# Kernel optimization log

Hardware: AMD Instinct MI355X
Metric: run time of the kernel (lower is better)

The kernel has to match this reference:

```python
import jax, jax.numpy as jnp
import numpy as np

SHIFT = 1e-09  # input_shift


def _patches(v, kh, kw):
    # v: (B, C, H, W) -> (B, C, kh*kw, Ho, Wo), VALID padding, stride 1
    B, C, H, W = v.shape
    Ho, Wo = H - kh + 1, W - kw + 1
    cols = [v[:, :, i:i + Ho, j:j + Wo] for i in range(kh) for j in range(kw)]
    return jnp.stack(cols, axis=2)


def setup_inputs() -> dict:
    key = jax.random.key(0)
    kx, k1k, k2k, kb = jax.random.split(key, 4)
    B, C, H, W = 32, 64, 64, 64
    kh, kw, F = 3, 3, 128
    x = jax.random.normal(kx, (B, C, H, W), dtype=jnp.float32)
    # log-domain kernels (learned params of the two Add modules)
    k1 = jax.random.normal(k1k, (kh, kw, C, F), dtype=jnp.float32) * 0.1
    k2 = jax.random.normal(k2k, (kh, kw, C, F), dtype=jnp.float32) * 0.1
    bias = jnp.zeros((F,), dtype=jnp.float32)
    return {"x": x, "k1": k1, "k2": k2, "bias": bias}


def reference(x, k1, k2, bias):
    kh, kw, C, F = k1.shape
    # Ln: log of ReLU'd patches (positive and negative parts of x)
    ep_pos = jnp.exp(jnp.log(jax.nn.relu(_patches(x, kh, kw)) + SHIFT))   # (B,C,kh*kw,Ho,Wo)
    ep_neg = jnp.exp(jnp.log(jax.nn.relu(_patches(-x, kh, kw)) + SHIFT))
    # Add + Exp + patch reduction: sum_p exp(ln_patch + k) == einsum(exp(ln_patch), exp(k))
    ek1 = jnp.exp(k1).reshape(kh * kw, C, F)
    ek2 = jnp.exp(k2).reshape(kh * kw, C, F)
    y11 = jnp.einsum('bckhw,kcf->bfhw', ep_pos, ek1)
    y12 = jnp.einsum('bckhw,kcf->bfhw', ep_pos, ek2)
    y21 = jnp.einsum('bckhw,kcf->bfhw', ep_neg, ek1)
    y22 = jnp.einsum('bckhw,kcf->bfhw', ep_neg, ek2)
    return y11 - y12 - y21 + y22 + bias[None, :, None, None]
```

## Files before the change

kernel.cpp:

```cpp
#include <hip/hip_runtime.h>
#include <hip/hip_bf16.h>

typedef __attribute__((ext_vector_type(4))) float f32x4;
typedef __attribute__((ext_vector_type(8))) short bf16x8;

static __device__ __forceinline__ unsigned short f2bf(float f) {
    unsigned int u = __float_as_uint(f);
    unsigned int r = (u + 0x7FFFu + ((u >> 16) & 1u)) >> 16;
    return (unsigned short)r;
}

__global__ __launch_bounds__(256) void wprep_kernel(const float* __restrict__ k1,
                                                    const float* __restrict__ k2,
                                                    unsigned short* __restrict__ wp) {
    int idx = blockIdx.x * 256 + threadIdx.x;
    if (idx >= 9 * 128 * 64) return;
    int c = idx & 63;
    int f = (idx >> 6) & 127;
    int p = idx >> 13;
    int src = (p * 64 + c) * 128 + f;
    float v = expf(k1[src]) - expf(k2[src]);
    wp[idx] = f2bf(v);
}

__global__ __launch_bounds__(256, 3) void conv_kernel(const float* __restrict__ x,
                                                      const unsigned short* __restrict__ wp,
                                                      const float* __restrict__ bias,
                                                      float* __restrict__ out) {
    __shared__ unsigned short xs[4 * 64 * 64];
    __shared__ unsigned short bs[128 * 64];

    int bid0 = blockIdx.x;
    int bid  = (bid0 & 7) * 124 + (bid0 >> 3);
    int b    = bid / 31;
    int tile = bid - b * 31;
    int oh0  = tile * 2;

    int tid  = threadIdx.x;
    int lane = tid & 63;
    const float* xb = x + b * (64 * 4096);
    const uint4* wp16 = (const uint4*)wp;

    uint4 wreg[4];
#pragma unroll
    for (int i2 = 0; i2 < 4; ++i2) wreg[i2] = wp16[i2 * 256 + tid];

    {
        int col = tid & 63;
        int u0  = tid >> 6;
#pragma unroll
        for (int j = 0; j < 8; ++j) {
            int u   = u0 + j * 4;
            int row = u >> 3;
            int cg  = u & 7;
            float v[8];
#pragma unroll
            for (int e = 0; e < 8; ++e)
                v[e] = xb[(cg * 8 + e) * 4096 + (oh0 + row) * 64 + col];
            uint4 pk;
            pk.x = (unsigned int)f2bf(v[0]) | ((unsigned int)f2bf(v[1]) << 16);
            pk.y = (unsigned int)f2bf(v[2]) | ((unsigned int)f2bf(v[3]) << 16);
            pk.z = (unsigned int)f2bf(v[4]) | ((unsigned int)f2bf(v[5]) << 16);
            pk.w = (unsigned int)f2bf(v[6]) | ((unsigned int)f2bf(v[7]) << 16);
            *(uint4*)(&xs[((row * 64 + col) << 6) + ((cg * 8) ^ ((col & 7) << 3))]) = pk;
        }
    }

    int wid = tid >> 6;
    int wr  = wid >> 1;
    int wc  = wid & 1;
    int lr  = lane & 15;
    int lk8 = (lane >> 4) << 3;

    f32x4 acc[4][4];
#pragma unroll
    for (int ni = 0; ni < 4; ++ni)
#pragma unroll
        for (int mi = 0; mi < 4; ++mi) acc[ni][mi] = (f32x4){0.f, 0.f, 0.f, 0.f};

#pragma unroll
    for (int p = 0; p < 9; ++p) {
        __syncthreads();
#pragma unroll
        for (int i2 = 0; i2 < 4; ++i2) {
            int q = i2 * 256 + tid;
            int f = q >> 3, cc = q & 7;
            *(uint4*)(&bs[f * 64 + ((cc * 8) ^ ((f & 7) << 3))]) = wreg[i2];
        }
        if (p < 8) {
#pragma unroll
            for (int i2 = 0; i2 < 4; ++i2) wreg[i2] = wp16[(p + 1) * 1024 + i2 * 256 + tid];
        }
        __syncthreads();
        const int ki = p / 3, kj = p % 3;
#pragma unroll
        for (int kb = 0; kb < 64; kb += 32) {
            int c0 = kb + lk8;
            bf16x8 af[4], bfr[4];
#pragma unroll
            for (int mi = 0; mi < 4; ++mi) {
                int col  = mi * 16 + lr + kj;
                int colc = col > 63 ? 63 : col;
                af[mi] = *(const bf16x8*)(&xs[(((wr + ki) * 64 + colc) << 6) + (c0 ^ ((colc & 7) << 3))]);
            }
#pragma unroll
            for (int ni = 0; ni < 4; ++ni) {
                int f = wc * 64 + ni * 16 + lr;
                bfr[ni] = *(const bf16x8*)(&bs[f * 64 + (c0 ^ ((f & 7) << 3))]);
            }
#pragma unroll
            for (int ni = 0; ni < 4; ++ni)
#pragma unroll
                for (int mi = 0; mi < 4; ++mi)
                    acc[ni][mi] = __builtin_amdgcn_mfma_f32_16x16x32_bf16(bfr[ni], af[mi], acc[ni][mi], 0, 0, 0);
        }
    }

    int oh = oh0 + wr;
    float* ob = out + b * (128 * 62 * 62);
#pragma unroll
    for (int ni = 0; ni < 4; ++ni) {
        int fb = wc * 64 + ni * 16 + ((lane >> 4) << 2);
        f32x4 bv4 = *(const f32x4*)(bias + fb);
#pragma unroll
        for (int t = 0; t < 4; ++t) {
            int f = fb + t;
            float* orow = ob + (f * 62 + oh) * 62;
#pragma unroll
            for (int mi = 0; mi < 4; ++mi) {
                int ow = mi * 16 + lr;
                if (ow < 62) orow[ow] = acc[ni][mi][t] + bv4[t];
            }
        }
    }
}

extern "C" void kernel_launch(void* const* d_in, const int* in_sizes, int n_in,
                              void* d_out, int out_size, void* d_ws, size_t ws_size,
                              hipStream_t stream) {
    const float* x    = (const float*)d_in[0];
    const float* k1   = (const float*)d_in[1];
    const float* k2   = (const float*)d_in[2];
    const float* bias = (const float*)d_in[3];
    float* out = (float*)d_out;

    unsigned short* wp = (unsigned short*)d_ws;

    hipLaunchKernelGGL(wprep_kernel, dim3(288), dim3(256), 0, stream, k1, k2, wp);
    hipLaunchKernelGGL(conv_kernel, dim3(992), dim3(256), 0, stream, x, wp, bias, out);
}
```

Measured before the change: 138.2 us.

## Load weight MFMA fragments directly from global into registers, drop LDS staging

The weight prep kernel now writes weights in a fragment-friendly layout (per tap, per half of the channel range, filter-major with 32 channels contiguous). Each lane of the conv kernel can then load its MFMA B operands straight from global or L2 into registers, double-buffered across the 9 taps. This removes the shared weight buffer and the two block barriers per tap. In exchange, each wave issues redundant global loads of the same weights and uses more registers, which may hurt occupancy.

```diff
diff --git a/kernel.cpp b/kernel.cpp
--- a/kernel.cpp
+++ b/kernel.cpp
@@ -4,31 +4,30 @@
 typedef __attribute__((ext_vector_type(4))) float f32x4;
 typedef __attribute__((ext_vector_type(8))) short bf16x8;
 
-static __device__ __forceinline__ unsigned short f2bf(float f) {
+static __device__ __forceinline__ unsigned int f2bf(float f) {
     unsigned int u = __float_as_uint(f);
-    unsigned int r = (u + 0x7FFFu + ((u >> 16) & 1u)) >> 16;
-    return (unsigned short)r;
+    return (u + 0x7FFFu + ((u >> 16) & 1u)) >> 16;
 }
 
 __global__ __launch_bounds__(256) void wprep_kernel(const float* __restrict__ k1,
                                                     const float* __restrict__ k2,
-                                                    unsigned short* __restrict__ wp) {
+                                                    unsigned short* __restrict__ wq) {
     int idx = blockIdx.x * 256 + threadIdx.x;
-    if (idx >= 9 * 128 * 64) return;
-    int c = idx & 63;
-    int f = (idx >> 6) & 127;
-    int p = idx >> 13;
-    int src = (p * 64 + c) * 128 + f;
+    if (idx >= 73728) return;
+    int f  = idx & 127;
+    int ch = (idx >> 7) & 31;
+    int kh = (idx >> 12) & 1;
+    int p  = idx >> 13;
+    int src = (p * 64 + kh * 32 + ch) * 128 + f;
     float v = expf(k1[src]) - expf(k2[src]);
-    wp[idx] = f2bf(v);
+    wq[((p * 2 + kh) * 128 + f) * 32 + ch] = (unsigned short)f2bf(v);
 }
 
 __global__ __launch_bounds__(256, 3) void conv_kernel(const float* __restrict__ x,
-                                                      const unsigned short* __restrict__ wp,
+                                                      const unsigned short* __restrict__ wq,
                                                       const float* __restrict__ bias,
                                                       float* __restrict__ out) {
     __shared__ unsigned short xs[4 * 64 * 64];
-    __shared__ unsigned short bs[128 * 64];
 
     int bid0 = blockIdx.x;
     int bid  = (bid0 & 7) * 124 + (bid0 >> 3);
@@ -38,19 +37,19 @@
 
     int tid  = threadIdx.x;
     int lane = tid & 63;
+    int wid  = tid >> 6;
+    int wr   = wid >> 1;
+    int wc   = wid & 1;
+    int lr   = lane & 15;
+    int hi   = lane >> 4;
+
     const float* xb = x + b * (64 * 4096);
-    const uint4* wp16 = (const uint4*)wp;
-
-    uint4 wreg[4];
-#pragma unroll
-    for (int i2 = 0; i2 < 4; ++i2) wreg[i2] = wp16[i2 * 256 + tid];
 
     {
         int col = tid & 63;
-        int u0  = tid >> 6;
 #pragma unroll
         for (int j = 0; j < 8; ++j) {
-            int u   = u0 + j * 4;
+            int u   = wid + j * 4;
             int row = u >> 3;
             int cg  = u & 7;
             float v[8];
@@ -58,19 +57,22 @@
             for (int e = 0; e < 8; ++e)
                 v[e] = xb[(cg * 8 + e) * 4096 + (oh0 + row) * 64 + col];
             uint4 pk;
-            pk.x = (unsigned int)f2bf(v[0]) | ((unsigned int)f2bf(v[1]) << 16);
-            pk.y = (unsigned int)f2bf(v[2]) | ((unsigned int)f2bf(v[3]) << 16);
-            pk.z = (unsigned int)f2bf(v[4]) | ((unsigned int)f2bf(v[5]) << 16);
-            pk.w = (unsigned int)f2bf(v[6]) | ((unsigned int)f2bf(v[7]) << 16);
+            pk.x = f2bf(v[0]) | (f2bf(v[1]) << 16);
+            pk.y = f2bf(v[2]) | (f2bf(v[3]) << 16);
+            pk.z = f2bf(v[4]) | (f2bf(v[5]) << 16);
+            pk.w = f2bf(v[6]) | (f2bf(v[7]) << 16);
             *(uint4*)(&xs[((row * 64 + col) << 6) + ((cg * 8) ^ ((col & 7) << 3))]) = pk;
         }
     }
 
-    int wid = tid >> 6;
-    int wr  = wid >> 1;
-    int wc  = wid & 1;
-    int lr  = lane & 15;
-    int lk8 = (lane >> 4) << 3;
+    const bf16x8* wg = (const bf16x8*)wq;
+    int fb0 = wc * 64 + lr;
+    bf16x8 wfrag[2][8];
+#pragma unroll
+    for (int kh = 0; kh < 2; ++kh)
+#pragma unroll
+        for (int ni = 0; ni < 4; ++ni)
+            wfrag[0][kh * 4 + ni] = wg[((kh) * 128 + fb0 + ni * 16) * 4 + hi];
 
     f32x4 acc[4][4];
 #pragma unroll
@@ -78,25 +80,23 @@
 #pragma unroll
         for (int mi = 0; mi < 4; ++mi) acc[ni][mi] = (f32x4){0.f, 0.f, 0.f, 0.f};
 
+    __syncthreads();
+
 #pragma unroll
     for (int p = 0; p < 9; ++p) {
-        __syncthreads();
-#pragma unroll
-        for (int i2 = 0; i2 < 4; ++i2) {
-            int q = i2 * 256 + tid;
-            int f = q >> 3, cc = q & 7;
-            *(uint4*)(&bs[f * 64 + ((cc * 8) ^ ((f & 7) << 3))]) = wreg[i2];
-        }
+        const int cur = p & 1, nxt = cur ^ 1;
         if (p < 8) {
 #pragma unroll
-            for (int i2 = 0; i2 < 4; ++i2) wreg[i2] = wp16[(p + 1) * 1024 + i2 * 256 + tid];
+            for (int kh = 0; kh < 2; ++kh)
+#pragma unroll
+                for (int ni = 0; ni < 4; ++ni)
+                    wfrag[nxt][kh * 4 + ni] = wg[(((p + 1) * 2 + kh) * 128 + fb0 + ni * 16) * 4 + hi];
         }
-        __syncthreads();
         const int ki = p / 3, kj = p % 3;
 #pragma unroll
-        for (int kb = 0; kb < 64; kb += 32) {
-            int c0 = kb + lk8;
-            bf16x8 af[4], bfr[4];
+        for (int kb = 0; kb < 2; ++kb) {
+            int c0 = kb * 32 + hi * 8;
+            bf16x8 af[4];
 #pragma unroll
             for (int mi = 0; mi < 4; ++mi) {
                 int col  = mi * 16 + lr + kj;
@@ -104,15 +104,11 @@
                 af[mi] = *(const bf16x8*)(&xs[(((wr + ki) * 64 + colc) << 6) + (c0 ^ ((colc & 7) << 3))]);
             }
 #pragma unroll
-            for (int ni = 0; ni < 4; ++ni) {
-                int f = wc * 64 + ni * 16 + lr;
-                bfr[ni] = *(const bf16x8*)(&bs[f * 64 + (c0 ^ ((f & 7) << 3))]);
-            }
-#pragma unroll
             for (int ni = 0; ni < 4; ++ni)
 #pragma unroll
                 for (int mi = 0; mi < 4; ++mi)
-                    acc[ni][mi] = __builtin_amdgcn_mfma_f32_16x16x32_bf16(bfr[ni], af[mi], acc[ni][mi], 0, 0, 0);
+                    acc[ni][mi] = __builtin_amdgcn_mfma_f32_16x16x32_bf16(
+                        wfrag[cur][kb * 4 + ni], af[mi], acc[ni][mi], 0, 0, 0);
         }
     }
 
@@ -120,12 +116,11 @@
     float* ob = out + b * (128 * 62 * 62);
 #pragma unroll
     for (int ni = 0; ni < 4; ++ni) {
-        int fb = wc * 64 + ni * 16 + ((lane >> 4) << 2);
+        int fb = wc * 64 + ni * 16 + (hi << 2);
         f32x4 bv4 = *(const f32x4*)(bias + fb);
 #pragma unroll
         for (int t = 0; t < 4; ++t) {
-            int f = fb + t;
-            float* orow = ob + (f * 62 + oh) * 62;
+            float* orow = ob + ((fb + t) * 62 + oh) * 62;
 #pragma unroll
             for (int mi = 0; mi < 4; ++mi) {
                 int ow = mi * 16 + lr;
@@ -144,8 +139,8 @@
     const float* bias = (const float*)d_in[3];
     float* out = (float*)d_out;
 
-    unsigned short* wp = (unsigned short*)d_ws;
+    unsigned short* wq = (unsigned short*)d_ws;
 
-    hipLaunchKernelGGL(wprep_kernel, dim3(288), dim3(256), 0, stream, k1, k2, wp);
-    hipLaunchKernelGGL(conv_kernel, dim3(992), dim3(256), 0, stream, x, wp, bias, out);
+    hipLaunchKernelGGL(wprep_kernel, dim3(288), dim3(256), 0, stream, k1, k2, wq);
+    hipLaunchKernelGGL(conv_kernel, dim3(992), dim3(256), 0, stream, x, wq, bias, out);
 }
```

After: 133.0 us. -3.8%, faster.
